# Kernel optimization log

Measured on AMD Instinct MI355X. Metric: run time of the kernel, lower is better.

## Reference

```python
import jax, jax.numpy as jnp
import numpy as np

B, L, D, H = 2, 2048, 2048, 16
DH = D // H  # 128


def setup_inputs() -> dict:
    key = jax.random.key(0)
    k1, k2 = jax.random.split(key)
    inputs = jax.random.normal(k1, (B, L, D), dtype=jnp.float32)
    # additive causal mask: 0 on/below diagonal, -inf above (matches typical usage)
    neg = jnp.finfo(jnp.float32).min
    causal = jnp.where(jnp.tril(jnp.ones((L, L), dtype=bool)), 0.0, neg)
    attn_mask = causal[None, None, :, :].astype(jnp.float32)
    # torch Linear(d, 3d, bias=False): y = x @ W.T; here W_qkv is stored as [d, 3d]
    W_qkv = jax.random.normal(k2, (D, 3 * D), dtype=jnp.float32) * (1.0 / np.sqrt(D))
    return {"inputs": inputs, "attn_mask": attn_mask, "W_qkv": W_qkv}


def reference(inputs, attn_mask, W_qkv):
    b, l, d = inputs.shape
    qkv = inputs @ W_qkv                       # [B, L, 3D]
    qkv = qkv.reshape(b, l, H, 3 * DH)         # [B, L, H, 3*dh]
    qkv = qkv.transpose(0, 2, 1, 3)            # [B, H, L, 3*dh]
    Q, K, V = jnp.split(qkv, 3, axis=-1)       # each [B, H, L, dh]
    scale = jnp.sqrt(jnp.float32(DH))
    scores = jnp.einsum("bhqd,bhkd->bhqk", Q, K) / scale
    scores = scores + attn_mask
    probs = jax.nn.softmax(scores, axis=-1)    # dropout is identity in eval / p=0
    out = jnp.einsum("bhqk,bhkd->bhqd", probs, V)
    out = out.transpose(0, 2, 1, 3).reshape(b, l, d)
    return out
```

## Files before the change

### kernel.cpp

```cpp
#include <hip/hip_runtime.h>

#define SEQL 2048
#define NHEAD 16
#define N3 6144
#define KDIM 2048

typedef __attribute__((ext_vector_type(8))) short bf16x8;
typedef __attribute__((ext_vector_type(4))) float f32x4;
typedef __attribute__((ext_vector_type(16))) float f32x16;
typedef __attribute__((ext_vector_type(4))) unsigned short us4;
typedef __attribute__((ext_vector_type(4))) float fl4;
typedef __attribute__((ext_vector_type(4))) unsigned int u32x4;

__device__ __forceinline__ unsigned short f2bf(float x) {
    unsigned u = __builtin_bit_cast(unsigned, x);
    u += 0x7fffu + ((u >> 16) & 1u);
    return (unsigned short)(u >> 16);
}

__device__ __forceinline__ void gload16(const void* g, void* l) {
    __builtin_amdgcn_global_load_lds(
        (const __attribute__((address_space(1))) unsigned int*)g,
        (__attribute__((address_space(3))) unsigned int*)l,
        16, 0, 0);
}

__device__ __forceinline__ unsigned cvtpk_bf16(float lo, float hi) {
    unsigned r;
    asm("v_cvt_pk_bf16_f32 %0, %1, %2" : "=v"(r) : "v"(lo), "v"(hi));
    return r;
}
__device__ __forceinline__ void plane32_swap(unsigned &a, unsigned &b) {
    asm("v_permlane32_swap_b32 %0, %1" : "+v"(a), "+v"(b));
}

__global__ __launch_bounds__(256) void k_prep(const float* __restrict__ X,
                                              const float* __restrict__ W,
                                              unsigned short* __restrict__ Xb,
                                              unsigned short* __restrict__ Wt) {
    __shared__ alignas(16) unsigned short Ts[64 * 68];
    int bid = blockIdx.x, t = threadIdx.x;
    if (bid < 2048) {
        int tid = bid * 256 + t;
        const fl4* in4 = (const fl4*)X;
        us4* out4 = (us4*)Xb;
#pragma unroll
        for (int j = 0; j < 4; ++j) {
            int idx = tid + j * 524288;
            fl4 v = in4[idx];
            us4 o;
            o.x = f2bf(v.x); o.y = f2bf(v.y); o.z = f2bf(v.z); o.w = f2bf(v.w);
            out4[idx] = o;
        }
    } else {
        int b2 = bid - 2048;
        int n0 = (b2 % 96) * 64, k0 = (b2 / 96) * 64;
        int r = t >> 2, c4 = t & 3;
#pragma unroll
        for (int j = 0; j < 4; ++j) {
            int c = (c4 + j * 4) * 4;
            fl4 v = *(const fl4*)&W[(size_t)(k0 + r) * N3 + n0 + c];
            Ts[r * 68 + c + 0] = f2bf(v.x);
            Ts[r * 68 + c + 1] = f2bf(v.y);
            Ts[r * 68 + c + 2] = f2bf(v.z);
            Ts[r * 68 + c + 3] = f2bf(v.w);
        }
        __syncthreads();
#pragma unroll
        for (int j = 0; j < 2; ++j) {
            int chunk = c4 + j * 4;
#pragma unroll
            for (int h = 0; h < 2; ++h) {
                us4 o;
                o.x = Ts[(chunk * 8 + h * 4 + 0) * 68 + r];
                o.y = Ts[(chunk * 8 + h * 4 + 1) * 68 + r];
                o.z = Ts[(chunk * 8 + h * 4 + 2) * 68 + r];
                o.w = Ts[(chunk * 8 + h * 4 + 3) * 68 + r];
                *(us4*)&Wt[(size_t)(n0 + r) * KDIM + k0 + chunk * 8 + h * 4] = o;
            }
        }
    }
}

__global__ __launch_bounds__(512, 4) void k_gemm_qkv(const unsigned short* __restrict__ Xb,
                                                     const unsigned short* __restrict__ Wt,
                                                     unsigned short* __restrict__ Qb,
                                                     unsigned short* __restrict__ Kb,
                                                     unsigned short* __restrict__ Vt) {
    __shared__ alignas(16) char smem[65536];
    int t = threadIdx.x;
    int wid = t >> 6, lane = t & 63, g = lane >> 4, l15 = lane & 15;
    int bid = blockIdx.x;
    bid = (bid & 7) * 96 + (bid >> 3);
    int tmi = bid & 31, tni = bid >> 5;
    int tm = tmi * 128, tn = tni * 256;
    const unsigned short* Abase = Xb + (size_t)tm * KDIM;
    const unsigned short* Bbase = Wt + (size_t)tn * KDIM;
    int wm = wid >> 2, wn = wid & 3;

    int mrA = t >> 3, psA = t & 7;
    int slA = psA ^ (mrA & 7);
    const unsigned short* a_src = Abase + (size_t)(mrA * 2 + (slA >> 2)) * KDIM + (slA & 3) * 8;
    int nr0 = t >> 3, sl0 = (t & 7) ^ (nr0 & 7);
    const unsigned short* b_src0 = Bbase + (size_t)(nr0 * 2 + (sl0 >> 2)) * KDIM + (sl0 & 3) * 8;
    int nr1 = 64 + (t >> 3), sl1 = (t & 7) ^ (nr1 & 7);
    const unsigned short* b_src1 = Bbase + (size_t)(nr1 * 2 + (sl1 >> 2)) * KDIM + (sl1 & 3) * 8;
    int awoff = wid * 1024 + lane * 16;

    int offA[4], offB[4];
#pragma unroll
    for (int q = 0; q < 4; ++q) {
        int ra = wm * 64 + q * 16 + l15;
        int mr = ra >> 1;
        offA[q] = mr * 128 + ((((ra & 1) * 4 + g) ^ (mr & 7)) << 4);
        int rb = wn * 64 + q * 16 + l15;
        int nr = rb >> 1;
        offB[q] = nr * 128 + ((((rb & 1) * 4 + g) ^ (nr & 7)) << 4);
    }

    f32x4 acc[4][4];
#pragma unroll
    for (int i = 0; i < 4; ++i)
#pragma unroll
        for (int j = 0; j < 4; ++j) acc[i][j] = (f32x4){0.f, 0.f, 0.f, 0.f};

    auto STAGE = [&](int tile) {
        int k0 = tile * 32;
        char* base = smem + (tile & 1) * 24576;
        gload16(a_src + k0, base + awoff);
        gload16(b_src0 + k0, base + 8192 + awoff);
        gload16(b_src1 + k0, base + 16384 + awoff);
    };

    STAGE(0); STAGE(1);
    asm volatile("s_waitcnt vmcnt(3)" ::: "memory");
    __builtin_amdgcn_s_barrier();
    asm volatile("" ::: "memory");

    for (int tt = 0; tt < 64; ++tt) {
        const char* base = smem + (tt & 1) * 24576;
        bf16x8 af[4], bfv[4];
#pragma unroll
        for (int q = 0; q < 4; ++q) {
            af[q]  = *(const bf16x8*)(base + offA[q]);
            bfv[q] = *(const bf16x8*)(base + 8192 + offB[q]);
        }
        __builtin_amdgcn_s_setprio(1);
#pragma unroll
        for (int i = 0; i < 4; ++i)
#pragma unroll
            for (int j = 0; j < 4; ++j)
                acc[i][j] = __builtin_amdgcn_mfma_f32_16x16x32_bf16(
                    af[i], bfv[j], acc[i][j], 0, 0, 0);
        __builtin_amdgcn_s_setprio(0);
        asm volatile("" ::: "memory");
        __builtin_amdgcn_s_barrier();
        asm volatile("" ::: "memory");
        if (tt < 62) {
            STAGE(tt + 2);
            asm volatile("s_waitcnt vmcnt(3)" ::: "memory");
        } else if (tt == 62) {
            asm volatile("s_waitcnt vmcnt(0)" ::: "memory");
        }
        __builtin_amdgcn_s_barrier();
        asm volatile("" ::: "memory");
    }

    int b = tm >> 11, lp0 = tm & 2047;
    const float qsc = 0.08838834764831845f * 1.44269504089f;
    int half_w = wn >> 1;
    int tyw = (2 * tni + half_w) % 3;
    char* Tw = smem + half_w * 32768;
#pragma unroll
    for (int fi = 0; fi < 4; ++fi)
#pragma unroll
        for (int bj = 0; bj < 4; ++bj) {
            int dl = (wn & 1) * 64 + bj * 16 + l15;
#pragma unroll
            for (int r = 0; r < 4; ++r) {
                int mm = wm * 64 + fi * 16 + g * 4 + r;
                float v = acc[fi][bj][r];
                unsigned short bv = f2bf(tyw == 0 ? v * qsc : v);
                int byte;
                if (tyw == 2)
                    byte = dl * 256 + ((((mm >> 3) ^ (dl & 15)) & 15) << 4) + (mm & 7) * 2;
                else
                    byte = mm * 256 + ((((dl >> 3) ^ (mm & 15)) & 15) << 4) + (dl & 7) * 2;
                *(unsigned short*)(Tw + byte) = bv;
            }
        }
    __syncthreads();
#pragma unroll
    for (int half = 0; half < 2; ++half) {
        int ty = (2 * tni + half) % 3;
        int hh = (tni * 256 + half * 128) / 384;
        const char* Tr = smem + half * 32768;
        if (ty == 2) {
#pragma unroll
            for (int i = 0; i < 4; ++i) {
                int id = i * 512 + t;
                int dv = id >> 4, c2 = id & 15;
                bf16x8 vv = *(const bf16x8*)(Tr + dv * 256 + (((c2 ^ (dv & 15)) & 15) << 4));
                int kt = (lp0 >> 6) + (c2 >> 3);
                *(bf16x8*)&Vt[(size_t)((b * NHEAD + hh) * 32 + kt) * 8192 + dv * 64 +
                              (c2 & 7) * 8] = vv;
            }
        } else {
            unsigned short* dst = (ty == 0) ? Qb : Kb;
#pragma unroll
            for (int i = 0; i < 4; ++i) {
                int id = i * 512 + t;
                int mm = id >> 4, cc = id & 15;
                bf16x8 vv = *(const bf16x8*)(Tr + mm * 256 + (((cc ^ (mm & 15)) & 15) << 4));
                *(bf16x8*)&dst[((size_t)(b * NHEAD + hh) * SEQL + lp0 + mm) * 128 + cc * 8] = vv;
            }
        }
    }
}

__global__ __launch_bounds__(256) void k_attn(const unsigned short* __restrict__ Qb,
                                              const unsigned short* __restrict__ Kb,
                                              const unsigned short* __restrict__ Vt,
                                              float* __restrict__ out) {
    __shared__ alignas(16) unsigned short Ks[64 * 128];
    __shared__ alignas(16) unsigned short Vs[128 * 64];
    __shared__ float Fx[4][32];
    int t = threadIdx.x, w = t >> 6, lane = t & 63;
    int l31 = lane & 31, hi = lane >> 5;
    int qi = 15 - (int)blockIdx.x;
    int bh = blockIdx.y;
    int qb = qi * 128;
    int qg = qb + w * 32 + l31;
    int qwmin = qb + w * 32, qwmax = qwmin + 31;

    bf16x8 qf[8];
    const unsigned short* Qp = Qb + (size_t)(bh * SEQL + qg) * 128;
#pragma unroll
    for (int ks = 0; ks < 8; ++ks)
        qf[ks] = *(const bf16x8*)(Qp + ks * 16 + hi * 8);

    f32x16 accO[4];
#pragma unroll
    for (int db = 0; db < 4; ++db)
#pragma unroll
        for (int e = 0; e < 16; ++e) accO[db][e] = 0.f;
    float mstate = -3.0e38f, lsum = 0.f;

    int nkv = 2 * qi + 2;
    for (int kt = 0; kt < nkv; ++kt) {
        int kv0 = kt * 64;
#pragma unroll
        for (int j = 0; j < 4; ++j) {
            int p = j * 4096 + t * 16;
            int rk = p >> 8;
            int sk = ((p >> 4) & 15) ^ (rk & 15);
            gload16(Kb + (size_t)(bh * SEQL + kv0 + rk) * 128 + sk * 8,
                    (char*)Ks + j * 4096 + w * 1024);
            int rv = p >> 7;
            int sv = ((p >> 4) & 7) ^ (rv & 7);
            gload16(Vt + ((size_t)(bh * 32 + (kv0 >> 6)) * 128 + rv) * 64 + sv * 8,
                    (char*)Vs + j * 4096 + w * 1024);
        }
        __syncthreads();

        if (kv0 <= qwmax) {
            f32x16 s[2];
#pragma unroll
            for (int blk = 0; blk < 2; ++blk)
#pragma unroll
                for (int e = 0; e < 16; ++e) s[blk][e] = 0.f;
#pragma unroll
            for (int ks = 0; ks < 8; ++ks) {
                int c = ks * 2 + hi;
#pragma unroll
                for (int blk = 0; blk < 2; ++blk) {
                    int row = blk * 32 + l31;
                    bf16x8 kf = *(const bf16x8*)((const char*)Ks + row * 256 +
                                                 (((c ^ (row & 15)) & 15) << 4));
                    s[blk] = __builtin_amdgcn_mfma_f32_32x32x16_bf16(kf, qf[ks], s[blk], 0, 0, 0);
                }
            }
            if (kv0 + 63 > qwmin) {
#pragma unroll
                for (int blk = 0; blk < 2; ++blk)
#pragma unroll
                    for (int r = 0; r < 16; ++r) {
                        int kvg = kv0 + blk * 32 + (r & 3) + 8 * (r >> 2) + 4 * hi;
                        if (kvg > qg) s[blk][r] = -3.0e38f;
                    }
            }
            float tmax = -3.0e38f;
#pragma unroll
            for (int blk = 0; blk < 2; ++blk)
#pragma unroll
                for (int r = 0; r < 16; ++r) tmax = fmaxf(tmax, s[blk][r]);
            tmax = fmaxf(tmax, __shfl_xor(tmax, 32));
            if (__any(tmax > mstate + 8.0f)) {
                float mnew = fmaxf(mstate, tmax);
                float fs = __builtin_amdgcn_exp2f(mstate - mnew);
                lsum *= fs;
                mstate = mnew;
                Fx[w][l31] = fs;
                f32x4 fv[4];
#pragma unroll
                for (int q4 = 0; q4 < 4; ++q4)
                    fv[q4] = *(const f32x4*)&Fx[w][q4 * 8 + 4 * hi];
#pragma unroll
                for (int db = 0; db < 4; ++db)
#pragma unroll
                    for (int r = 0; r < 16; ++r)
                        accO[db][r] *= fv[r >> 2][r & 3];
            }
            float ps = 0.f;
#pragma unroll
            for (int blk = 0; blk < 2; ++blk)
#pragma unroll
                for (int r = 0; r < 16; ++r) {
                    float p = __builtin_amdgcn_exp2f(s[blk][r] - mstate);
                    s[blk][r] = p;
                    ps += p;
                }
            ps += __shfl_xor(ps, 32);
            lsum += ps;
            unsigned pa[4][4];
#pragma unroll
            for (int blk = 0; blk < 2; ++blk)
#pragma unroll
                for (int hf = 0; hf < 2; ++hf) {
                    int o = hf * 8;
                    unsigned d0 = cvtpk_bf16(s[blk][o + 0], s[blk][o + 1]);
                    unsigned d2 = cvtpk_bf16(s[blk][o + 4], s[blk][o + 5]);
                    plane32_swap(d0, d2);
                    unsigned d1 = cvtpk_bf16(s[blk][o + 2], s[blk][o + 3]);
                    unsigned d3 = cvtpk_bf16(s[blk][o + 6], s[blk][o + 7]);
                    plane32_swap(d1, d3);
                    pa[blk * 2 + hf][0] = d0; pa[blk * 2 + hf][1] = d1;
                    pa[blk * 2 + hf][2] = d2; pa[blk * 2 + hf][3] = d3;
                }
#pragma unroll
            for (int ksv = 0; ksv < 4; ++ksv) {
                u32x4 pu = {pa[ksv][0], pa[ksv][1], pa[ksv][2], pa[ksv][3]};
                bf16x8 paf = __builtin_bit_cast(bf16x8, pu);
                int c = ksv * 2 + hi;
#pragma unroll
                for (int db = 0; db < 4; ++db) {
                    int rv = db * 32 + l31;
                    bf16x8 vf = *(const bf16x8*)((const char*)Vs + rv * 128 +
                                                 (((c ^ (rv & 7)) & 7) << 4));
                    accO[db] = __builtin_amdgcn_mfma_f32_32x32x16_bf16(paf, vf, accO[db], 0, 0, 0);
                }
            }
        }
        __syncthreads();
    }
    float inv = 1.0f / lsum;
    Fx[w][l31] = inv;
    f32x4 iv[4];
#pragma unroll
    for (int q4 = 0; q4 < 4; ++q4)
        iv[q4] = *(const f32x4*)&Fx[w][q4 * 8 + 4 * hi];
    int b = bh >> 4, h = bh & 15;
    float* ob = out + (size_t)(b * SEQL + qb + w * 32) * 2048 + h * 128;
#pragma unroll
    for (int db = 0; db < 4; ++db)
#pragma unroll
        for (int r = 0; r < 16; ++r) {
            int qr = (r & 3) + 8 * (r >> 2) + 4 * hi;
            ob[(size_t)qr * 2048 + db * 32 + l31] = accO[db][r] * iv[r >> 2][r & 3];
        }
}

extern "C" void kernel_launch(void* const* d_in, const int* in_sizes, int n_in,
                              void* d_out, int out_size, void* d_ws, size_t ws_size,
                              hipStream_t stream) {
    const float* x = (const float*)d_in[0];
    const float* w = (const float*)d_in[2];
    float* out = (float*)d_out;
    char* ws = (char*)d_ws;
    unsigned short* Xb = (unsigned short*)(ws);
    unsigned short* Wt = (unsigned short*)(ws + 16777216);
    unsigned short* Qb = (unsigned short*)(ws + 41943040);
    unsigned short* Kb = (unsigned short*)(ws + 58720256);
    unsigned short* Vt = (unsigned short*)(ws + 75497472);

    hipLaunchKernelGGL(k_prep, dim3(5120), dim3(256), 0, stream, x, w, Xb, Wt);
    hipLaunchKernelGGL(k_gemm_qkv, dim3(768), dim3(512), 0, stream, Xb, Wt, Qb, Kb, Vt);
    hipLaunchKernelGGL(k_attn, dim3(16, 32), dim3(256), 0, stream, Qb, Kb, Vt, out);
}
```

Baseline: 362.6 us.

## Pair causal query tiles per attention block for balanced work and XCD-aware mapping

The attention kernel now uses 128-thread blocks with 64-row query tiles. Each block handles two tiles, qa=31-pr and pr, across a fixed 33 KV iterations, so every block does the same causal workload. Block IDs are mapped so that all blocks for one (batch, head) land on the same XCD, which should improve L2 reuse of K/V. The W transpose in the prep kernel also now does one 16-byte store per chunk instead of two 8-byte stores. The trade-off is half as many waves per block, each sharing the K/V loads, and an extra output write partway through the loop.

```diff
diff --git a/kernel.cpp b/kernel.cpp
--- a/kernel.cpp
+++ b/kernel.cpp
@@ -6,6 +6,7 @@
 #define KDIM 2048
 
 typedef __attribute__((ext_vector_type(8))) short bf16x8;
+typedef __attribute__((ext_vector_type(8))) unsigned short us8;
 typedef __attribute__((ext_vector_type(4))) float f32x4;
 typedef __attribute__((ext_vector_type(16))) float f32x16;
 typedef __attribute__((ext_vector_type(4))) unsigned short us4;
@@ -68,16 +69,12 @@
         __syncthreads();
 #pragma unroll
         for (int j = 0; j < 2; ++j) {
-            int chunk = c4 + j * 4;
-#pragma unroll
-            for (int h = 0; h < 2; ++h) {
-                us4 o;
-                o.x = Ts[(chunk * 8 + h * 4 + 0) * 68 + r];
-                o.y = Ts[(chunk * 8 + h * 4 + 1) * 68 + r];
-                o.z = Ts[(chunk * 8 + h * 4 + 2) * 68 + r];
-                o.w = Ts[(chunk * 8 + h * 4 + 3) * 68 + r];
-                *(us4*)&Wt[(size_t)(n0 + r) * KDIM + k0 + chunk * 8 + h * 4] = o;
-            }
+            int chunk = c4 * 2 + j;
+            us8 o;
+#pragma unroll
+            for (int e = 0; e < 8; ++e)
+                o[e] = Ts[(chunk * 8 + e) * 68 + r];
+            *(us8*)&Wt[(size_t)(n0 + r) * KDIM + k0 + chunk * 8] = o;
         }
     }
 }
@@ -218,26 +215,33 @@
     }
 }
 
-__global__ __launch_bounds__(256) void k_attn(const unsigned short* __restrict__ Qb,
-                                              const unsigned short* __restrict__ Kb,
-                                              const unsigned short* __restrict__ Vt,
-                                              float* __restrict__ out) {
+__global__ __launch_bounds__(128, 2) void k_attn(const unsigned short* __restrict__ Qb,
+                                                 const unsigned short* __restrict__ Kb,
+                                                 const unsigned short* __restrict__ Vt,
+                                                 float* __restrict__ out) {
     __shared__ alignas(16) unsigned short Ks[64 * 128];
     __shared__ alignas(16) unsigned short Vs[128 * 64];
-    __shared__ float Fx[4][32];
+    __shared__ float Fx[2][32];
     int t = threadIdx.x, w = t >> 6, lane = t & 63;
     int l31 = lane & 31, hi = lane >> 5;
-    int qi = 15 - (int)blockIdx.x;
-    int bh = blockIdx.y;
-    int qb = qi * 128;
-    int qg = qb + w * 32 + l31;
-    int qwmin = qb + w * 32, qwmax = qwmin + 31;
+    int pid = blockIdx.x;
+    int xcd = pid & 7, q3 = pid >> 3;
+    int bh = (q3 >> 4) * 8 + xcd;
+    int pr = q3 & 15;
+    int qa = 31 - pr, qb2 = pr;
+    int n1 = qa + 1;
+
+    int qt = qa;
+    int qg = qt * 64 + w * 32 + l31;
+    int qwmin = qt * 64 + w * 32, qwmax = qwmin + 31;
 
     bf16x8 qf[8];
-    const unsigned short* Qp = Qb + (size_t)(bh * SEQL + qg) * 128;
-#pragma unroll
-    for (int ks = 0; ks < 8; ++ks)
-        qf[ks] = *(const bf16x8*)(Qp + ks * 16 + hi * 8);
+    {
+        const unsigned short* Qp = Qb + (size_t)(bh * SEQL + qg) * 128;
+#pragma unroll
+        for (int ks = 0; ks < 8; ++ks)
+            qf[ks] = *(const bf16x8*)(Qp + ks * 16 + hi * 8);
+    }
 
     f32x16 accO[4];
 #pragma unroll
@@ -245,23 +249,56 @@
 #pragma unroll
         for (int e = 0; e < 16; ++e) accO[db][e] = 0.f;
     float mstate = -3.0e38f, lsum = 0.f;
-
-    int nkv = 2 * qi + 2;
-    for (int kt = 0; kt < nkv; ++kt) {
-        int kv0 = kt * 64;
-#pragma unroll
-        for (int j = 0; j < 4; ++j) {
-            int p = j * 4096 + t * 16;
+    int b_out = bh >> 4, h_out = bh & 15;
+
+    auto writeO = [&](int qtv) {
+        float inv = 1.0f / lsum;
+        Fx[w][l31] = inv;
+        f32x4 iv[4];
+#pragma unroll
+        for (int q4 = 0; q4 < 4; ++q4)
+            iv[q4] = *(const f32x4*)&Fx[w][q4 * 8 + 4 * hi];
+        float* ob = out + (size_t)(b_out * SEQL + qtv * 64 + w * 32) * 2048 + h_out * 128;
+#pragma unroll
+        for (int db = 0; db < 4; ++db)
+#pragma unroll
+            for (int r = 0; r < 16; ++r) {
+                int qr = (r & 3) + 8 * (r >> 2) + 4 * hi;
+                ob[(size_t)qr * 2048 + db * 32 + l31] = accO[db][r] * iv[r >> 2][r & 3];
+            }
+    };
+
+    for (int it = 0; it < 33; ++it) {
+        int kv0 = (it < n1 ? it : it - n1) * 64;
+#pragma unroll
+        for (int j = 0; j < 8; ++j) {
+            int p = j * 2048 + t * 16;
             int rk = p >> 8;
             int sk = ((p >> 4) & 15) ^ (rk & 15);
             gload16(Kb + (size_t)(bh * SEQL + kv0 + rk) * 128 + sk * 8,
-                    (char*)Ks + j * 4096 + w * 1024);
+                    (char*)Ks + j * 2048 + w * 1024);
             int rv = p >> 7;
             int sv = ((p >> 4) & 7) ^ (rv & 7);
             gload16(Vt + ((size_t)(bh * 32 + (kv0 >> 6)) * 128 + rv) * 64 + sv * 8,
-                    (char*)Vs + j * 4096 + w * 1024);
+                    (char*)Vs + j * 2048 + w * 1024);
         }
         __syncthreads();
+
+        if (it == n1) {
+            writeO(qa);
+            qt = qb2;
+            qg = qt * 64 + w * 32 + l31;
+            qwmin = qt * 64 + w * 32; qwmax = qwmin + 31;
+            const unsigned short* Qp = Qb + (size_t)(bh * SEQL + qg) * 128;
+#pragma unroll
+            for (int ks = 0; ks < 8; ++ks)
+                qf[ks] = *(const bf16x8*)(Qp + ks * 16 + hi * 8);
+#pragma unroll
+            for (int db = 0; db < 4; ++db)
+#pragma unroll
+                for (int e = 0; e < 16; ++e) accO[db][e] = 0.f;
+            mstate = -3.0e38f; lsum = 0.f;
+        }
 
         if (kv0 <= qwmax) {
             f32x16 s[2];
@@ -353,21 +390,7 @@
         }
         __syncthreads();
     }
-    float inv = 1.0f / lsum;
-    Fx[w][l31] = inv;
-    f32x4 iv[4];
-#pragma unroll
-    for (int q4 = 0; q4 < 4; ++q4)
-        iv[q4] = *(const f32x4*)&Fx[w][q4 * 8 + 4 * hi];
-    int b = bh >> 4, h = bh & 15;
-    float* ob = out + (size_t)(b * SEQL + qb + w * 32) * 2048 + h * 128;
-#pragma unroll
-    for (int db = 0; db < 4; ++db)
-#pragma unroll
-        for (int r = 0; r < 16; ++r) {
-            int qr = (r & 3) + 8 * (r >> 2) + 4 * hi;
-            ob[(size_t)qr * 2048 + db * 32 + l31] = accO[db][r] * iv[r >> 2][r & 3];
-        }
+    writeO(qb2);
 }
 
 extern "C" void kernel_launch(void* const* d_in, const int* in_sizes, int n_in,
@@ -385,5 +408,5 @@
 
     hipLaunchKernelGGL(k_prep, dim3(5120), dim3(256), 0, stream, x, w, Xb, Wt);
     hipLaunchKernelGGL(k_gemm_qkv, dim3(768), dim3(512), 0, stream, Xb, Wt, Qb, Kb, Vt);
-    hipLaunchKernelGGL(k_attn, dim3(16, 32), dim3(256), 0, stream, Qb, Kb, Vt, out);
-}
+    hipLaunchKernelGGL(k_attn, dim3(512), dim3(128), 0, stream, Qb, Kb, Vt, out);
+}
```

New measurement: 342.4 us. -5.6%, faster.
